# Kernel tuning notes

Measured on AMD Instinct MI355X. Metric: run time of the kernel, lower is better.

Reference implementation:

```python
import jax, jax.numpy as jnp
import numpy as np

RX = 1024
RY = 1024
F = 4
HID = 64
N = 2097152


def setup_inputs() -> dict:
    key = jax.random.key(0)
    ks = jax.random.split(key, 8)
    x = jax.random.uniform(ks[0], (N, 3), dtype=jnp.float32)  # (id, u, v) in [0,1)
    emb = jax.random.uniform(ks[1], (RX * RY, F), dtype=jnp.float32) * 2.0 - 1.0
    din = 1 + F  # id feature + interpolated grid feature
    w1 = jax.random.normal(ks[2], (din, HID), dtype=jnp.float32) / np.sqrt(din)
    b1 = jnp.zeros((HID,), dtype=jnp.float32)
    w2 = jax.random.normal(ks[3], (HID, HID), dtype=jnp.float32) / np.sqrt(HID)
    b2 = jnp.zeros((HID,), dtype=jnp.float32)
    w3 = jax.random.normal(ks[4], (HID, 3), dtype=jnp.float32) / np.sqrt(HID)
    b3 = jnp.zeros((3,), dtype=jnp.float32)
    return {"x": x, "emb": emb, "w1": w1, "b1": b1, "w2": w2, "b2": b2, "w3": w3, "b3": b3}


def _grid_features(uv, emb):
    u, v = uv[:, 0], uv[:, 1]
    # vertex ids of bounding cell, faithful to the torch edge handling
    x0 = (u * RX).astype(jnp.int32)
    x0 = jnp.where(x0 == RX, 0, x0)          # wrap exactly-1.0 to 0
    x1 = jnp.where(x0 + 1 == RX, RX - 1, x0 + 1)
    y0 = (v * RY).astype(jnp.int32)
    y1 = jnp.where(y0 + 1 == RY, RY - 1, y0 + 1)
    # weights computed AFTER the x0 wrap, as in the original
    wx = (u * RX - x0.astype(jnp.float32))[:, None]
    wy = (v * RY - y0.astype(jnp.float32))[:, None]
    # four gathers from the flat [RX*RY, F] table (row index = y*RX + x)
    v00 = emb[y0 * RX + x0]
    v10 = emb[y0 * RX + x1]
    v01 = emb[y1 * RX + x0]
    v11 = emb[y1 * RX + x1]
    vup = v00 * (1.0 - wx) + v10 * wx
    vdn = v01 * (1.0 - wx) + v11 * wx
    return vup * (1.0 - wy) + vdn * wy


def reference(x, emb, w1, b1, w2, b2, w3, b3):
    idf = x[:, :1]
    dgf = _grid_features(x[:, 1:3], emb)
    h = jnp.concatenate([idf, dgf], axis=1)   # [N, 5]
    h = jax.nn.relu(h @ w1 + b1)
    h = jax.nn.relu(h @ w2 + b2)
    return jax.nn.sigmoid(h @ w3 + b3)        # [N, 3]
```

## Files before the change

### kernel.cpp

```cpp
#include <hip/hip_runtime.h>
#include <hip/hip_bf16.h>


typedef __attribute__((ext_vector_type(8))) short bf16x8;
typedef __attribute__((ext_vector_type(4))) float f32x4;
typedef __attribute__((ext_vector_type(2))) unsigned int u32x2;
typedef __attribute__((ext_vector_type(4))) unsigned int u32x4;
typedef unsigned long long u64t;

#define HID 64

static __device__ __forceinline__ unsigned short f2bf(float f) {
    __hip_bfloat16 h = __float2bfloat16(f);
    return __builtin_bit_cast(unsigned short, h);
}
static __device__ __forceinline__ unsigned cvt_pk_bf16(float a, float b) {
    unsigned r;
    asm("v_cvt_pk_bf16_f32 %0, %1, %2" : "=v"(r) : "v"(a), "v"(b));
    return r;
}
static __device__ __forceinline__ void lds_fence() {
    asm volatile("s_waitcnt lgkmcnt(0)" ::: "memory");
}
#define MFMA16(a,b,c) __builtin_amdgcn_mfma_f32_16x16x32_bf16((a),(b),(c),0,0,0)

static __device__ __forceinline__ f32x4 unpk(u64t q) {
    unsigned lo = (unsigned)q, hi = (unsigned)(q >> 32);
    f32x4 r;
    r[0] = __builtin_bit_cast(float, lo << 16);
    r[1] = __builtin_bit_cast(float, lo & 0xFFFF0000u);
    r[2] = __builtin_bit_cast(float, hi << 16);
    r[3] = __builtin_bit_cast(float, hi & 0xFFFF0000u);
    return r;
}
static __device__ __forceinline__ bf16x8 pack_pair(f32x4 lo, f32x4 hi) {
    u32x4 w;
    w[0] = cvt_pk_bf16(fmaxf(lo[0], 0.f), fmaxf(lo[1], 0.f));
    w[1] = cvt_pk_bf16(fmaxf(lo[2], 0.f), fmaxf(lo[3], 0.f));
    w[2] = cvt_pk_bf16(fmaxf(hi[0], 0.f), fmaxf(hi[1], 0.f));
    w[3] = cvt_pk_bf16(fmaxf(hi[2], 0.f), fmaxf(hi[3], 0.f));
    return __builtin_bit_cast(bf16x8, w);
}

struct TFrags {
    bf16x8 a1[4];
    bf16x8 a2[4][2];
    bf16x8 a3[2];
    f32x4  bias2[4];
    f32x4  bias3;
};

static __device__ __forceinline__ void build_tfrags(
    float* Wst, int tid, int cl, int kg,
    const float* __restrict__ w1, const float* __restrict__ b1,
    const float* __restrict__ w2, const float* __restrict__ b2,
    const float* __restrict__ w3, const float* __restrict__ b3, TFrags& F)
{
    {
        const f32x4* w2v = (const f32x4*)w2;
        f32x4* Wv = (f32x4*)Wst;
        #pragma unroll
        for (int i = 0; i < 4; ++i) Wv[tid + 256 * i] = w2v[tid + 256 * i];
        for (int idx = tid; idx < 320; idx += 256) Wst[4096 + idx] = w1[idx];
        if (tid < 64)  Wst[4416 + tid] = b1[tid];
        if (tid < 192) Wst[4480 + tid] = w3[tid];
        if (tid < 64)  Wst[4672 + tid] = b2[tid];
        if (tid < 3)   Wst[4736 + tid] = b3[tid];
    }
    __syncthreads();

    #pragma unroll
    for (int mt = 0; mt < 4; ++mt) {
        bf16x8 f = {};
        if (kg == 0) {
            int hid = mt * 16 + cl;
            #pragma unroll
            for (int j = 0; j < 5; ++j) f[j] = (short)f2bf(Wst[4096 + j * 64 + hid]);
            f[5] = (short)f2bf(Wst[4416 + hid]);
        }
        F.a1[mt] = f;
    }
    #pragma unroll
    for (int ks = 0; ks < 2; ++ks) {
        #pragma unroll
        for (int mt2 = 0; mt2 < 4; ++mt2) {
            bf16x8 f;
            #pragma unroll
            for (int j = 0; j < 8; ++j) {
                int kap = (2 * ks + (j >> 2)) * 16 + kg * 4 + (j & 3);
                f[j] = (short)f2bf(Wst[kap * 64 + mt2 * 16 + cl]);
            }
            F.a2[mt2][ks] = f;
        }
        bf16x8 f3 = {};
        if (cl < 3) {
            #pragma unroll
            for (int j = 0; j < 8; ++j) {
                int kap = (2 * ks + (j >> 2)) * 16 + kg * 4 + (j & 3);
                f3[j] = (short)f2bf(Wst[4480 + kap * 3 + cl]);
            }
        }
        F.a3[ks] = f3;
    }
    #pragma unroll
    for (int mt2 = 0; mt2 < 4; ++mt2) {
        f32x4 b;
        #pragma unroll
        for (int r = 0; r < 4; ++r) b[r] = Wst[4672 + mt2 * 16 + kg * 4 + r];
        F.bias2[mt2] = b;
    }
    {
        f32x4 b = {};
        if (kg == 0) { b[0] = Wst[4736]; b[1] = Wst[4737]; b[2] = Wst[4738]; }
        F.bias3 = b;
    }
    __syncthreads();
}

__global__ __launch_bounds__(256) void conv_emb(const f32x4* __restrict__ emb,
                                                u32x2* __restrict__ tab) {
    int t = blockIdx.x * 256 + threadIdx.x;
    f32x4 v = emb[t];
    u32x2 p = {cvt_pk_bf16(v[0], v[1]), cvt_pk_bf16(v[2], v[3])};
    tab[t] = p;
}

template<int BT>
__global__ __launch_bounds__(256, 3)
void dgn_fused(const float* __restrict__ x, const void* __restrict__ tabv,
               const float* __restrict__ w1, const float* __restrict__ b1,
               const float* __restrict__ w2, const float* __restrict__ b2,
               const float* __restrict__ w3, const float* __restrict__ b3,
               float* __restrict__ out, int n)
{
    __shared__ __align__(16) float Wst[4768];

    const int tid = threadIdx.x, wid = tid >> 6, lane = tid & 63;
    const int cl = lane & 15, kg = lane >> 4;

    TFrags F;
    build_tfrags(Wst, tid, cl, kg, w1, b1, w2, b2, w3, b3, F);

    u32x4* Xf = (u32x4*)Wst + wid * 64;

    const u64t*  __restrict__ tab8 = (const u64t*)tabv;
    const f32x4* __restrict__ tabf = (const f32x4*)tabv;

    const int SP   = gridDim.x * 256;
    const int blk0 = blockIdx.x * 256;
    if (blk0 >= n) return;
    const int iters = (n - blk0 + SP - 1) / SP;
    const int wb0   = blk0 + wid * 64;

    #define LOADX(I, A, B, C) { int pt_ = wb0 + (I) * SP + lane;                \
        int pc_ = pt_ < n ? pt_ : 0; const float* xp_ = x + 3 * pc_;            \
        A = xp_[0]; B = xp_[1]; C = xp_[2]; }

    #define GISSUE(U, V, T, Fv, WX, WY) {                                       \
        float uf_ = (U) * 1024.f, vf_ = (V) * 1024.f;                           \
        int x0_ = (int)uf_; if (x0_ == 1024) x0_ = 0;                           \
        int x1_ = (x0_ + 1 == 1024) ? 1023 : x0_ + 1;                           \
        int y0_ = (int)vf_;                                                     \
        WX = uf_ - (float)x0_; WY = vf_ - (float)y0_;                           \
        if (y0_ > 1023) y0_ = 1023;                                             \
        int y1_ = (y0_ + 1 > 1023) ? 1023 : y0_ + 1;                            \
        int r0_ = y0_ << 10, r1_ = y1_ << 10;                                   \
        if (BT) { T[0] = tab8[r0_ + x0_]; T[1] = tab8[r0_ + x1_];               \
                  T[2] = tab8[r1_ + x0_]; T[3] = tab8[r1_ + x1_]; }             \
        else    { Fv[0] = tabf[r0_ + x0_]; Fv[1] = tabf[r0_ + x1_];             \
                  Fv[2] = tabf[r1_ + x0_]; Fv[3] = tabf[r1_ + x1_]; } }

    u64t  cT[4] = {};  f32x4 cF[4] = {};
    float cwx, cwy, cid;
    float nx0, nx1, nx2;
    {
        float p0, p1, p2;
        LOADX(0, p0, p1, p2);
        GISSUE(p1, p2, cT, cF, cwx, cwy);
        cid = p0;
        LOADX(1, nx0, nx1, nx2);
    }

    for (int i = 0; i < iters; ++i) {
        u64t  tT[4] = {};  f32x4 tF[4] = {};
        float twx = 0.f, twy = 0.f, tcid = 0.f;
        const bool more = (i + 1 < iters);
        if (more) {
            GISSUE(nx1, nx2, tT, tF, twx, twy);
            tcid = nx0;
            int nix = (i + 2 < iters) ? i + 2 : i + 1;
            LOADX(nix, nx0, nx1, nx2);
        }

        f32x4 A, B, C, D;
        if (BT) { A = unpk(cT[0]); B = unpk(cT[1]); C = unpk(cT[2]); D = unpk(cT[3]); }
        else    { A = cF[0]; B = cF[1]; C = cF[2]; D = cF[3]; }
        f32x4 up = A + (B - A) * cwx;
        f32x4 dn = C + (D - C) * cwx;
        f32x4 g  = up + (dn - up) * cwy;

        u32x4 inq = {cvt_pk_bf16(cid, g[0]), cvt_pk_bf16(g[1], g[2]),
                     cvt_pk_bf16(g[3], 1.0f), 0u};
        Xf[lane] = inq;
        lds_fence();
        u32x4 bq0 = Xf[0 * 16 + cl];
        u32x4 bq1 = Xf[1 * 16 + cl];
        u32x4 bq2 = Xf[2 * 16 + cl];
        u32x4 bq3 = Xf[3 * 16 + cl];

        const int tb = wb0 + i * SP;
        #pragma unroll
        for (int nt = 0; nt < 4; ++nt) {
            u32x4 bqs = (nt == 0) ? bq0 : (nt == 1) ? bq1 : (nt == 2) ? bq2 : bq3;
            bf16x8 bb = __builtin_bit_cast(bf16x8, bqs);

            f32x4 c1_0 = {}, c1_1 = {}, c1_2 = {}, c1_3 = {};
            c1_0 = MFMA16(F.a1[0], bb, c1_0);
            c1_1 = MFMA16(F.a1[1], bb, c1_1);
            c1_2 = MFMA16(F.a1[2], bb, c1_2);
            c1_3 = MFMA16(F.a1[3], bb, c1_3);

            bf16x8 p0 = pack_pair(c1_0, c1_1);
            bf16x8 p1 = pack_pair(c1_2, c1_3);

            f32x4 c2_0 = F.bias2[0], c2_1 = F.bias2[1],
                  c2_2 = F.bias2[2], c2_3 = F.bias2[3];
            c2_0 = MFMA16(F.a2[0][0], p0, c2_0); c2_0 = MFMA16(F.a2[0][1], p1, c2_0);
            c2_1 = MFMA16(F.a2[1][0], p0, c2_1); c2_1 = MFMA16(F.a2[1][1], p1, c2_1);
            c2_2 = MFMA16(F.a2[2][0], p0, c2_2); c2_2 = MFMA16(F.a2[2][1], p1, c2_2);
            c2_3 = MFMA16(F.a2[3][0], p0, c2_3); c2_3 = MFMA16(F.a2[3][1], p1, c2_3);

            bf16x8 q0 = pack_pair(c2_0, c2_1);
            bf16x8 q1 = pack_pair(c2_2, c2_3);

            f32x4 c3 = F.bias3;
            c3 = MFMA16(F.a3[0], q0, c3);
            c3 = MFMA16(F.a3[1], q1, c3);

            if (kg == 0) {
                int pt = tb + nt * 16 + cl;
                if (pt < n) {
                    #pragma unroll
                    for (int r = 0; r < 3; ++r) {
                        float s = __builtin_amdgcn_rcpf(1.0f + __expf(-c3[r]));
                        out[pt * 3 + r] = s;
                    }
                }
            }
        }

        if (more) {
            #pragma unroll
            for (int j = 0; j < 4; ++j) { cT[j] = tT[j]; cF[j] = tF[j]; }
            cwx = twx; cwy = twy; cid = tcid;
        }
    }
    #undef LOADX
    #undef GISSUE
}

extern "C" void kernel_launch(void* const* d_in, const int* in_sizes, int n_in,
                              void* d_out, int out_size, void* d_ws, size_t ws_size,
                              hipStream_t stream) {
    const float* x   = (const float*)d_in[0];
    const float* emb = (const float*)d_in[1];
    const float* w1  = (const float*)d_in[2];
    const float* b1  = (const float*)d_in[3];
    const float* w2  = (const float*)d_in[4];
    const float* b2  = (const float*)d_in[5];
    const float* w3  = (const float*)d_in[6];
    const float* b3  = (const float*)d_in[7];
    float* out = (float*)d_out;

    int n = in_sizes[0] / 3;
    int nblk = (n + 255) / 256;
    if (nblk > 768) nblk = 768;

    const size_t tab_bytes = (size_t)8 * 1024 * 1024;
    if (ws_size >= tab_bytes) {
        conv_emb<<<dim3(4096), dim3(256), 0, stream>>>((const f32x4*)emb, (u32x2*)d_ws);
        dgn_fused<1><<<dim3(nblk), dim3(256), 0, stream>>>(
            x, d_ws, w1, b1, w2, b2, w3, b3, out, n);
    } else {
        dgn_fused<0><<<dim3(nblk), dim3(256), 0, stream>>>(
            x, emb, w1, b1, w2, b2, w3, b3, out, n);
    }
}
```

Before: 74.09 us.

## Duplicate next-row texels in bf16 table to halve bilinear gathers

The preprocessing kernel now builds a 16-byte-per-texel bf16 table holding each texel's four features together with those of the texel one row below. The main kernel can then fetch all four bilinear corners with two 16-byte gathers instead of four 8-byte gathers, cutting random memory transactions. The table grows to 16 MB, so the conversion pass writes twice as much and the gather footprint is larger. Occupancy hint raised from 3 to 4 blocks per CU and the grid cap raised from 768 to 1024 blocks.

```diff
diff --git a/kernel.cpp b/kernel.cpp
--- a/kernel.cpp
+++ b/kernel.cpp
@@ -24,8 +24,7 @@
 }
 #define MFMA16(a,b,c) __builtin_amdgcn_mfma_f32_16x16x32_bf16((a),(b),(c),0,0,0)
 
-static __device__ __forceinline__ f32x4 unpk(u64t q) {
-    unsigned lo = (unsigned)q, hi = (unsigned)(q >> 32);
+static __device__ __forceinline__ f32x4 unpk2(unsigned lo, unsigned hi) {
     f32x4 r;
     r[0] = __builtin_bit_cast(float, lo << 16);
     r[1] = __builtin_bit_cast(float, lo & 0xFFFF0000u);
@@ -117,16 +116,21 @@
     __syncthreads();
 }
 
-__global__ __launch_bounds__(256) void conv_emb(const f32x4* __restrict__ emb,
-                                                u32x2* __restrict__ tab) {
+__global__ __launch_bounds__(256) void conv_dup(const f32x4* __restrict__ emb,
+                                                u32x4* __restrict__ tabd) {
     int t = blockIdx.x * 256 + threadIdx.x;
-    f32x4 v = emb[t];
-    u32x2 p = {cvt_pk_bf16(v[0], v[1]), cvt_pk_bf16(v[2], v[3])};
-    tab[t] = p;
+    int y = t >> 10;
+    int y1 = (y + 1 > 1023) ? 1023 : y + 1;
+    int x = t & 1023;
+    f32x4 a = emb[(y << 10) + x];
+    f32x4 b = emb[(y1 << 10) + x];
+    u32x4 p = {cvt_pk_bf16(a[0], a[1]), cvt_pk_bf16(a[2], a[3]),
+               cvt_pk_bf16(b[0], b[1]), cvt_pk_bf16(b[2], b[3])};
+    tabd[t] = p;
 }
 
 template<int BT>
-__global__ __launch_bounds__(256, 3)
+__global__ __launch_bounds__(256, 4)
 void dgn_fused(const float* __restrict__ x, const void* __restrict__ tabv,
                const float* __restrict__ w1, const float* __restrict__ b1,
                const float* __restrict__ w2, const float* __restrict__ b2,
@@ -143,7 +147,7 @@
 
     u32x4* Xf = (u32x4*)Wst + wid * 64;
 
-    const u64t*  __restrict__ tab8 = (const u64t*)tabv;
+    const u32x4* __restrict__ tabd = (const u32x4*)tabv;
     const f32x4* __restrict__ tabf = (const f32x4*)tabv;
 
     const int SP   = gridDim.x * 256;
@@ -156,45 +160,50 @@
         int pc_ = pt_ < n ? pt_ : 0; const float* xp_ = x + 3 * pc_;            \
         A = xp_[0]; B = xp_[1]; C = xp_[2]; }
 
-    #define GISSUE(U, V, T, Fv, WX, WY) {                                       \
+    #define GISSUE(U, V, T0, T1, Fv, WX, WY) {                                  \
         float uf_ = (U) * 1024.f, vf_ = (V) * 1024.f;                           \
         int x0_ = (int)uf_; if (x0_ == 1024) x0_ = 0;                           \
         int x1_ = (x0_ + 1 == 1024) ? 1023 : x0_ + 1;                           \
         int y0_ = (int)vf_;                                                     \
         WX = uf_ - (float)x0_; WY = vf_ - (float)y0_;                           \
         if (y0_ > 1023) y0_ = 1023;                                             \
-        int y1_ = (y0_ + 1 > 1023) ? 1023 : y0_ + 1;                            \
-        int r0_ = y0_ << 10, r1_ = y1_ << 10;                                   \
-        if (BT) { T[0] = tab8[r0_ + x0_]; T[1] = tab8[r0_ + x1_];               \
-                  T[2] = tab8[r1_ + x0_]; T[3] = tab8[r1_ + x1_]; }             \
-        else    { Fv[0] = tabf[r0_ + x0_]; Fv[1] = tabf[r0_ + x1_];             \
-                  Fv[2] = tabf[r1_ + x0_]; Fv[3] = tabf[r1_ + x1_]; } }
-
-    u64t  cT[4] = {};  f32x4 cF[4] = {};
+        int r0_ = y0_ << 10;                                                    \
+        if (BT) { T0 = tabd[r0_ + x0_]; T1 = tabd[r0_ + x1_]; }                 \
+        else {                                                                  \
+            int y1_ = (y0_ + 1 > 1023) ? 1023 : y0_ + 1;                        \
+            int r1_ = y1_ << 10;                                                \
+            Fv[0] = tabf[r0_ + x0_]; Fv[1] = tabf[r0_ + x1_];                   \
+            Fv[2] = tabf[r1_ + x0_]; Fv[3] = tabf[r1_ + x1_]; } }
+
+    u32x4 cT0 = {}, cT1 = {};
+    f32x4 cF[4] = {};
     float cwx, cwy, cid;
     float nx0, nx1, nx2;
     {
         float p0, p1, p2;
         LOADX(0, p0, p1, p2);
-        GISSUE(p1, p2, cT, cF, cwx, cwy);
+        GISSUE(p1, p2, cT0, cT1, cF, cwx, cwy);
         cid = p0;
         LOADX(1, nx0, nx1, nx2);
     }
 
     for (int i = 0; i < iters; ++i) {
-        u64t  tT[4] = {};  f32x4 tF[4] = {};
+        u32x4 tT0 = {}, tT1 = {};
+        f32x4 tF[4] = {};
         float twx = 0.f, twy = 0.f, tcid = 0.f;
         const bool more = (i + 1 < iters);
         if (more) {
-            GISSUE(nx1, nx2, tT, tF, twx, twy);
+            GISSUE(nx1, nx2, tT0, tT1, tF, twx, twy);
             tcid = nx0;
             int nix = (i + 2 < iters) ? i + 2 : i + 1;
             LOADX(nix, nx0, nx1, nx2);
         }
 
         f32x4 A, B, C, D;
-        if (BT) { A = unpk(cT[0]); B = unpk(cT[1]); C = unpk(cT[2]); D = unpk(cT[3]); }
-        else    { A = cF[0]; B = cF[1]; C = cF[2]; D = cF[3]; }
+        if (BT) {
+            A = unpk2(cT0[0], cT0[1]);  C = unpk2(cT0[2], cT0[3]);
+            B = unpk2(cT1[0], cT1[1]);  D = unpk2(cT1[2], cT1[3]);
+        } else { A = cF[0]; B = cF[1]; C = cF[2]; D = cF[3]; }
         f32x4 up = A + (B - A) * cwx;
         f32x4 dn = C + (D - C) * cwx;
         f32x4 g  = up + (dn - up) * cwy;
@@ -250,8 +259,9 @@
         }
 
         if (more) {
-            #pragma unroll
-            for (int j = 0; j < 4; ++j) { cT[j] = tT[j]; cF[j] = tF[j]; }
+            cT0 = tT0; cT1 = tT1;
+            #pragma unroll
+            for (int j = 0; j < 4; ++j) cF[j] = tF[j];
             cwx = twx; cwy = twy; cid = tcid;
         }
     }
@@ -274,11 +284,11 @@
 
     int n = in_sizes[0] / 3;
     int nblk = (n + 255) / 256;
-    if (nblk > 768) nblk = 768;
-
-    const size_t tab_bytes = (size_t)8 * 1024 * 1024;
+    if (nblk > 1024) nblk = 1024;
+
+    const size_t tab_bytes = (size_t)16 * 1024 * 1024;
     if (ws_size >= tab_bytes) {
-        conv_emb<<<dim3(4096), dim3(256), 0, stream>>>((const f32x4*)emb, (u32x2*)d_ws);
+        conv_dup<<<dim3(4096), dim3(256), 0, stream>>>((const f32x4*)emb, (u32x4*)d_ws);
         dgn_fused<1><<<dim3(nblk), dim3(256), 0, stream>>>(
             x, d_ws, w1, b1, w2, b2, w3, b3, out, n);
     } else {
```

New measurement: 92.30 us. 1.25x slower.
